# Performance work log

Hardware: AMD Instinct MI355X
Metric: run time of the kernel (lower is better)

## Reference

```python
import jax, jax.numpy as jnp
import numpy as np

EMBED_DIM = 1024
NUM_HEADS = 16
HEAD_DIM = EMBED_DIM // NUM_HEADS


def setup_inputs() -> dict:
    key = jax.random.key(0)
    ks = jax.random.split(key, 8)
    B, S, D = 2, 2048, EMBED_DIM
    scale = 1.0 / np.sqrt(D)
    return {
        "query": jax.random.normal(ks[0], (B, S, D), dtype=jnp.float32),
        "key": jax.random.normal(ks[1], (B, S, D), dtype=jnp.float32),
        "value": jax.random.normal(ks[2], (B, S, D), dtype=jnp.float32),
        "Wq": jax.random.normal(ks[3], (D, D), dtype=jnp.float32) * scale,
        "Wk": jax.random.normal(ks[4], (D, D), dtype=jnp.float32) * scale,
        "Wv": jax.random.normal(ks[5], (D, D), dtype=jnp.float32) * scale,
        "Wo": jax.random.normal(ks[6], (D, D), dtype=jnp.float32) * scale,
        "attention_mask": jax.random.randint(ks[7], (B, S), 0, 2, dtype=jnp.int32),
    }


def reference(query, key, value, Wq, Wk, Wv, Wo, attention_mask):
    B, Sq, D = query.shape
    Sk = key.shape[1]
    H, hd = NUM_HEADS, HEAD_DIM
    # linear projections (no bias), split into heads: [B, H, S, hd]
    q = (query @ Wq).reshape(B, Sq, H, hd).transpose(0, 2, 1, 3)
    k = (key @ Wk).reshape(B, Sk, H, hd).transpose(0, 2, 1, 3)
    v = (value @ Wv).reshape(B, Sk, H, hd).transpose(0, 2, 1, 3)
    # scaled dot-product scores: [B, H, Sq, Sk]; scale uses head_dim (post-split key dim)
    scores = jnp.einsum("bhqd,bhkd->bhqk", q, k) / jnp.sqrt(jnp.float32(hd))
    # padding mask [B, Sk] broadcast to [B, 1, 1, Sk]; 0 -> -inf
    mask = attention_mask[:, None, None, :]
    scores = jnp.where(mask == 0, -jnp.inf, scores)
    weights = jax.nn.softmax(scores, axis=-1)
    out = jnp.einsum("bhqk,bhkd->bhqd", weights, v)  # [B, H, Sq, hd]
    out = out.transpose(0, 2, 1, 3).reshape(B, Sq, D)
    return out @ Wo
```

## Files before the change

kernel.cpp:

```cpp
#include <hip/hip_runtime.h>
#include <hip/hip_bf16.h>

typedef short bf16x8 __attribute__((ext_vector_type(8)));
typedef float f32x4 __attribute__((ext_vector_type(4)));

#define S_LEN 2048
#define NHEAD 16
#define DM 1024

#if __has_builtin(__builtin_amdgcn_exp2f)
#define EXP2(x) __builtin_amdgcn_exp2f(x)
#else
#define EXP2(x) exp2f(x)
#endif

__device__ __forceinline__ short f2bf(float f) {
  union { float f; unsigned u; } x; x.f = f;
  unsigned r = x.u + 0x7fffu + ((x.u >> 16) & 1u);
  return (short)(r >> 16);
}

__device__ __forceinline__ unsigned cvt_pk_bf16(float lo, float hi) {
  unsigned r;
  asm("v_cvt_pk_bf16_f32 %0, %1, %2" : "=v"(r) : "v"(lo), "v"(hi));
  return r;
}

__device__ __forceinline__ void pl32swap(unsigned& a, unsigned& b) {
#if __has_builtin(__builtin_amdgcn_permlane32_swap)
  auto r = __builtin_amdgcn_permlane32_swap(a, b, false, false);
  a = r[0]; b = r[1];
#else
  asm volatile("v_permlane32_swap_b32 %0, %1" : "+v"(a), "+v"(b));
#endif
}
__device__ __forceinline__ void pl16swap(unsigned& a, unsigned& b) {
#if __has_builtin(__builtin_amdgcn_permlane16_swap)
  auto r = __builtin_amdgcn_permlane16_swap(a, b, false, false);
  a = r[0]; b = r[1];
#else
  asm volatile("v_permlane16_swap_b32 %0, %1" : "+v"(a), "+v"(b));
#endif
}

__device__ __forceinline__ void gload16(const void* g, void* l) {
  __builtin_amdgcn_global_load_lds(
      (const __attribute__((address_space(1))) void*)g,
      (__attribute__((address_space(3))) void*)l, 16, 0, 0);
}

__global__ __launch_bounds__(256) void wtrans(const float* __restrict__ Wq, const float* __restrict__ Wk,
                                              const float* __restrict__ Wv, const float* __restrict__ Wo,
                                              const int* __restrict__ mask,
                                              short* Tq, short* Tk, short* Tv, short* To, short* Mb) {
  const int z = blockIdx.z;
  const int tid = threadIdx.x;
  if (z == 4) {
    if (blockIdx.y == 0 && blockIdx.x < 16) {
      int i = blockIdx.x * 256 + tid;
      Mb[i] = mask[i] ? (short)0x3F80 : (short)0;
    }
    return;
  }
  const float* W = (z == 0) ? Wq : (z == 1) ? Wk : (z == 2) ? Wv : Wo;
  short* T = (z == 0) ? Tq : (z == 1) ? Tk : (z == 2) ? Tv : To;
  __shared__ short Tl[64][72];
  const int k0 = blockIdx.x * 64, n0 = blockIdx.y * 64;
  const int r = tid >> 2, c0 = (tid & 3) * 16;
#pragma unroll
  for (int j = 0; j < 4; j++) {
    float4 v = *(const float4*)&W[(size_t)(k0 + r) * DM + n0 + c0 + 4 * j];
    Tl[r][c0 + 4 * j + 0] = f2bf(v.x);
    Tl[r][c0 + 4 * j + 1] = f2bf(v.y);
    Tl[r][c0 + 4 * j + 2] = f2bf(v.z);
    Tl[r][c0 + 4 * j + 3] = f2bf(v.w);
  }
  __syncthreads();
  bf16x8 o0, o1;
#pragma unroll
  for (int j = 0; j < 8; j++) { o0[j] = Tl[c0 + j][r]; o1[j] = Tl[c0 + 8 + j][r]; }
  *(bf16x8*)&T[(size_t)(n0 + r) * DM + k0 + c0] = o0;
  *(bf16x8*)&T[(size_t)(n0 + r) * DM + k0 + c0 + 8] = o1;
}

__global__ __launch_bounds__(256) void xcvt(const float* __restrict__ q, const float* __restrict__ k,
                                            const float* __restrict__ v,
                                            short* xq, short* xk, short* xv) {
  const int z = blockIdx.y;
  const float* src = (z == 0) ? q : (z == 1) ? k : v;
  short* dst = (z == 0) ? xq : (z == 1) ? xk : xv;
  const size_t base = ((size_t)blockIdx.x * 256 + threadIdx.x) * 16;
  float4 a = *(const float4*)&src[base];
  float4 b = *(const float4*)&src[base + 4];
  float4 c = *(const float4*)&src[base + 8];
  float4 d = *(const float4*)&src[base + 12];
  bf16x8 o0, o1;
  o0[0] = f2bf(a.x); o0[1] = f2bf(a.y); o0[2] = f2bf(a.z); o0[3] = f2bf(a.w);
  o0[4] = f2bf(b.x); o0[5] = f2bf(b.y); o0[6] = f2bf(b.z); o0[7] = f2bf(b.w);
  o1[0] = f2bf(c.x); o1[1] = f2bf(c.y); o1[2] = f2bf(c.z); o1[3] = f2bf(c.w);
  o1[4] = f2bf(d.x); o1[5] = f2bf(d.y); o1[6] = f2bf(d.z); o1[7] = f2bf(d.w);
  *(bf16x8*)&dst[base] = o0;
  *(bf16x8*)&dst[base + 8] = o1;
}

template<int CM>
__global__ __launch_bounds__(256) void gemm3(const short* __restrict__ A, const short* __restrict__ Bt,
                                             void* __restrict__ Cp, int M, int N, int K,
                                             const int* __restrict__ mask) {
  __shared__ __align__(16) short Al[2][128 * 64];
  __shared__ __align__(16) short Bl[2][64 * 64];
  const int tid = threadIdx.x;
  const int lane = tid & 63, w = tid >> 6;
  const int wm = w >> 1, wn = w & 1;
  const int lr = lane & 15, g = lane >> 4;

  const int flat = blockIdx.y * gridDim.x + blockIdx.x;
  const int nwg = gridDim.x * gridDim.y;
  const int wid = (flat & 7) * (nwg >> 3) + (flat >> 3);
  const int bx = wid % gridDim.x, by = wid / gridDim.x;
  const int m0 = by * 128, n0 = bx * 64;

  f32x4 acc[4][2];
#pragma unroll
  for (int i = 0; i < 4; i++)
#pragma unroll
    for (int j = 0; j < 2; j++) acc[i][j] = (f32x4){0.f, 0.f, 0.f, 0.f};

  const int srow = lane >> 3;
  const int sch = (lane & 7) ^ (srow & 7);
  const short* gA = A + (size_t)(m0 + w * 32 + srow) * K + 8 * sch;
  const short* gB = Bt + (size_t)(n0 + w * 16 + srow) * K + 8 * sch;

#define STAGE(buf, kk)                                                              \
  do {                                                                              \
    _Pragma("unroll") for (int c = 0; c < 4; c++)                                   \
        gload16(gA + (size_t)c * 8 * K + (kk), &Al[buf][(w * 32 + c * 8) * 64]);    \
    _Pragma("unroll") for (int c = 0; c < 2; c++)                                   \
        gload16(gB + (size_t)c * 8 * K + (kk), &Bl[buf][(w * 16 + c * 8) * 64]);    \
  } while (0)

  const int nsteps = K >> 6;
  STAGE(0, 0);
  int buf = 0;
  for (int t = 0; t < nsteps; t++) {
    __syncthreads();
    if (t + 1 < nsteps) STAGE(buf ^ 1, (t + 1) << 6);
#pragma unroll
    for (int kc = 0; kc < 2; kc++) {
      bf16x8 af[4], bfr[2];
#pragma unroll
      for (int mt = 0; mt < 4; mt++) {
        int row = wm * 64 + mt * 16 + lr;
        af[mt] = *(const bf16x8*)&Al[buf][row * 64 + 8 * ((kc * 4 + g) ^ (lr & 7))];
      }
#pragma unroll
      for (int nt = 0; nt < 2; nt++) {
        int row = wn * 32 + nt * 16 + lr;
        bfr[nt] = *(const bf16x8*)&Bl[buf][row * 64 + 8 * ((kc * 4 + g) ^ (lr & 7))];
      }
      __builtin_amdgcn_s_setprio(1);
#pragma unroll
      for (int mt = 0; mt < 4; mt++)
#pragma unroll
        for (int nt = 0; nt < 2; nt++)
          acc[mt][nt] = __builtin_amdgcn_mfma_f32_16x16x32_bf16(af[mt], bfr[nt], acc[mt][nt], 0, 0, 0);
      __builtin_amdgcn_s_setprio(0);
    }
    buf ^= 1;
  }
#undef STAGE

#pragma unroll
  for (int mt = 0; mt < 4; mt++)
#pragma unroll
    for (int nt = 0; nt < 2; nt++) {
      if (CM == 0) {
#pragma unroll
        for (int r = 0; r < 4; r++) {
          int row = m0 + wm * 64 + mt * 16 + g * 4 + r;
          int col = n0 + wn * 32 + nt * 16 + lr;
          ((float*)Cp)[(size_t)row * N + col] = acc[mt][nt][r];
        }
      } else if (CM == 1 || CM == 3) {
        const float scale = (CM == 3) ? 0.18033688011f : 1.f;
#pragma unroll
        for (int r = 0; r < 4; r++) {
          int row = m0 + wm * 64 + mt * 16 + g * 4 + r;
          int col = n0 + wn * 32 + nt * 16 + lr;
          int b = row >> 11, s = row & (S_LEN - 1);
          int h = col >> 6, d = col & 63;
          ((short*)Cp)[(((size_t)(b * NHEAD + h)) * S_LEN + s) * 64 + d] = f2bf(acc[mt][nt][r] * scale);
        }
      } else {
#pragma unroll
        for (int r = 0; r < 4; r++) {
          int row = m0 + wm * 64 + mt * 16 + g * 4 + r;
          int col = n0 + wn * 32 + nt * 16 + lr;
          int h = row >> 6, d = row & 63;
          int b = col >> 11, s = col & (S_LEN - 1);
          float v = acc[mt][nt][r];
          if (CM == 4) v = mask[b * S_LEN + s] ? v : 0.f;
          ((short*)Cp)[(((size_t)(b * NHEAD + h)) * 64 + d) * S_LEN + s] = f2bf(v);
        }
      }
    }
}

template<int AM, int BMODE, int CM>
__global__ __launch_bounds__(256) void gemm2(const void* __restrict__ Ap, const void* __restrict__ Bp,
                                             void* __restrict__ Cp, int M, int N, int K) {
  __shared__ __align__(16) short Al[128][72];
  __shared__ __align__(16) short Bl[64][72];
  const int tid = threadIdx.x;
  const int lane = tid & 63, w = tid >> 6;
  const int wm = w >> 1, wn = w & 1;
  const int lr = lane & 15, g = lane >> 4;
  const int m0 = blockIdx.y * 128, n0 = blockIdx.x * 64;

  f32x4 acc[4][2];
#pragma unroll
  for (int i = 0; i < 4; i++)
// ... 68 lines not shown
      for (int j = 0; j < 2; j++) *(bf16x8*)&Bl[br][bc + 8 * j] = lb8[j];
    } else {
#pragma unroll
      for (int j = 0; j < 4; j++) {
        float4 v = lb[j];
        Bl[bc + 4 * j + 0][br] = f2bf(v.x);
        Bl[bc + 4 * j + 1][br] = f2bf(v.y);
        Bl[bc + 4 * j + 2][br] = f2bf(v.z);
        Bl[bc + 4 * j + 3][br] = f2bf(v.w);
      }
    }
    __syncthreads();
    if (t + 1 < nsteps) { LOADA((t + 1) << 6); LOADB((t + 1) << 6); }
#pragma unroll
    for (int kc = 0; kc < 2; kc++) {
      bf16x8 af[4], bfr[2];
#pragma unroll
      for (int mt = 0; mt < 4; mt++) af[mt] = *(const bf16x8*)&Al[wm * 64 + mt * 16 + lr][kc * 32 + g * 8];
#pragma unroll
      for (int nt = 0; nt < 2; nt++) bfr[nt] = *(const bf16x8*)&Bl[wn * 32 + nt * 16 + lr][kc * 32 + g * 8];
#pragma unroll
      for (int mt = 0; mt < 4; mt++)
#pragma unroll
        for (int nt = 0; nt < 2; nt++)
          acc[mt][nt] = __builtin_amdgcn_mfma_f32_16x16x32_bf16(af[mt], bfr[nt], acc[mt][nt], 0, 0, 0);
    }
  }
#undef LOADA
#undef LOADB

#pragma unroll
  for (int mt = 0; mt < 4; mt++)
#pragma unroll
    for (int nt = 0; nt < 2; nt++)
#pragma unroll
      for (int r = 0; r < 4; r++) {
        int row = m0 + wm * 64 + mt * 16 + g * 4 + r;
        int col = n0 + wn * 32 + nt * 16 + lr;
        if (CM == 0) {
          ((float*)Cp)[(size_t)row * N + col] = acc[mt][nt][r];
        } else if (CM == 1 || CM == 3) {
          float v = (CM == 3) ? acc[mt][nt][r] * 0.18033688011f : acc[mt][nt][r];
          int b = row >> 11, s = row & (S_LEN - 1);
          int h = col >> 6, d = col & 63;
          ((short*)Cp)[(((size_t)(b * NHEAD + h)) * S_LEN + s) * 64 + d] = f2bf(v);
        } else {
          int h = row >> 6, d = row & 63;
          int b = col >> 11, s = col & (S_LEN - 1);
          ((short*)Cp)[(((size_t)(b * NHEAD + h)) * 64 + d) * S_LEN + s] = f2bf(acc[mt][nt][r]);
        }
      }
}

__global__ __launch_bounds__(256, 4) void attn8(const short* __restrict__ Qb,
                                                const short* __restrict__ Kb,
                                                const short* __restrict__ VbT,
                                                const short* __restrict__ Mb,
                                                short* __restrict__ Ob) {
  __shared__ __align__(16) short Kl[2][64][64];
  __shared__ __align__(16) short Vl[2][64][64];

  const int tid = threadIdx.x;
  const int lane = tid & 63, w = tid >> 6;
  const int lr = lane & 15, g = lane >> 4;

  const int flat = blockIdx.y * gridDim.x + blockIdx.x;
  const int wid = (flat & 7) * 128 + (flat >> 3);
  const int qblk = wid & 31, bh = wid >> 5;
  const int b = bh >> 4, h = bh & 15;
  const int qbase = qblk * 64;
  const size_t hoff = (size_t)bh * S_LEN * 64;

  bf16x8 qf[2];
#pragma unroll
  for (int kh = 0; kh < 2; kh++)
    qf[kh] = *(const bf16x8*)&Qb[hoff + (size_t)(qbase + w * 16 + lr) * 64 + kh * 32 + g * 8];

  f32x4 o_acc[4];
  f32x4 o_l = (f32x4){0.f, 0.f, 0.f, 0.f};
#pragma unroll
  for (int dg = 0; dg < 4; dg++) o_acc[dg] = (f32x4){0.f, 0.f, 0.f, 0.f};

  const short* Mbb = Mb + b * S_LEN;
  const int srow = lane >> 3;
  const int sch = (lane & 7) ^ (srow & 7);
  const short* gK = Kb + hoff + (size_t)(w * 16 + srow) * 64 + 8 * sch;
  const short* gV = VbT + hoff + (size_t)(w * 16 + srow) * S_LEN + 8 * sch;

#define STAGEKV(buf, kb)                                                         \
  do {                                                                           \
    _Pragma("unroll") for (int c = 0; c < 2; c++)                                \
        gload16(gK + (size_t)(kb + c * 8) * 64, &Kl[buf][w * 16 + c * 8][0]);    \
    _Pragma("unroll") for (int c = 0; c < 2; c++)                                \
        gload16(gV + (size_t)c * 8 * S_LEN + (kb), &Vl[buf][w * 16 + c * 8][0]); \
  } while (0)

  const int NT = S_LEN / 64;
  STAGEKV(0, 0);
  int buf = 0;

  for (int t = 0; t < NT; t++) {
    const int kb = t * 64;
    bf16x8 mf0 = *(const bf16x8*)&Mbb[kb + g * 8];
    bf16x8 mf1 = *(const bf16x8*)&Mbb[kb + 32 + g * 8];
    __syncthreads();
    if (t + 1 < NT) STAGEKV(buf ^ 1, kb + 64);

    f32x4 s[4];
#pragma unroll
    for (int nt = 0; nt < 4; nt++) s[nt] = (f32x4){0.f, 0.f, 0.f, 0.f};
    __builtin_amdgcn_s_setprio(1);
#pragma unroll
    for (int nt = 0; nt < 4; nt++) {
      bf16x8 k0 = *(const bf16x8*)&Kl[buf][nt * 16 + lr][8 * (g ^ (lr & 7))];
      bf16x8 k1 = *(const bf16x8*)&Kl[buf][nt * 16 + lr][8 * ((4 + g) ^ (lr & 7))];
      s[nt] = __builtin_amdgcn_mfma_f32_16x16x32_bf16(k0, qf[0], s[nt], 0, 0, 0);
      s[nt] = __builtin_amdgcn_mfma_f32_16x16x32_bf16(k1, qf[1], s[nt], 0, 0, 0);
    }
    __builtin_amdgcn_s_setprio(0);

    unsigned W0[4], W1[4];
#pragma unroll
    for (int nt = 0; nt < 4; nt++) {
      float p0 = EXP2(s[nt][0]);
      float p1 = EXP2(s[nt][1]);
      float p2 = EXP2(s[nt][2]);
      float p3 = EXP2(s[nt][3]);
      W0[nt] = cvt_pk_bf16(p0, p1);
      W1[nt] = cvt_pk_bf16(p2, p3);
    }

    bf16x8 pf[2];
#pragma unroll
    for (int kh = 0; kh < 2; kh++) {
      unsigned a0 = W0[2 * kh], b0 = W0[2 * kh + 1];
      unsigned a1 = W1[2 * kh], b1 = W1[2 * kh + 1];
      pl32swap(a0, b0); pl16swap(a0, b0);
      pl32swap(a1, b1); pl16swap(a1, b1);
      union { unsigned u[4]; bf16x8 v; } pk;
      pk.u[0] = a0; pk.u[1] = a1; pk.u[2] = b0; pk.u[3] = b1;
      pf[kh] = pk.v;
    }

    __builtin_amdgcn_s_setprio(1);
#pragma unroll
    for (int dg = 0; dg < 4; dg++) {
      bf16x8 v0 = *(const bf16x8*)&Vl[buf][dg * 16 + lr][8 * (g ^ (lr & 7))];
      bf16x8 v1 = *(const bf16x8*)&Vl[buf][dg * 16 + lr][8 * ((4 + g) ^ (lr & 7))];
      o_acc[dg] = __builtin_amdgcn_mfma_f32_16x16x32_bf16(pf[0], v0, o_acc[dg], 0, 0, 0);
      o_acc[dg] = __builtin_amdgcn_mfma_f32_16x16x32_bf16(pf[1], v1, o_acc[dg], 0, 0, 0);
    }
    o_l = __builtin_amdgcn_mfma_f32_16x16x32_bf16(pf[0], mf0, o_l, 0, 0, 0);
    o_l = __builtin_amdgcn_mfma_f32_16x16x32_bf16(pf[1], mf1, o_l, 0, 0, 0);
    __builtin_amdgcn_s_setprio(0);
    buf ^= 1;
  }
#undef STAGEKV

#pragma unroll
  for (int r = 0; r < 4; r++) {
    float inv = 1.f / o_l[r];
    int qr = qbase + w * 16 + 4 * g + r;
#pragma unroll
    for (int dg = 0; dg < 4; dg++) {
      int col = h * 64 + dg * 16 + lr;
      Ob[((size_t)b * S_LEN + qr) * DM + col] = f2bf(o_acc[dg][r] * inv);
    }
  }
}

__global__ __launch_bounds__(256, 4) void attn7(const short* __restrict__ Qb,
                                                const short* __restrict__ Kb,
                                                const short* __restrict__ VbT,
                                                const int* __restrict__ mask,
                                                short* __restrict__ Ob) {
  __shared__ __align__(16) short Kl[2][64][64];
  __shared__ __align__(16) short Vl[2][64][64];

  const int tid = threadIdx.x;
  const int lane = tid & 63, w = tid >> 6;
  const int lr = lane & 15, g = lane >> 4;

  const int flat = blockIdx.y * gridDim.x + blockIdx.x;
  const int wid = (flat & 7) * 128 + (flat >> 3);
  const int qblk = wid & 31, bh = wid >> 5;
  const int b = bh >> 4, h = bh & 15;
  const int qbase = qblk * 64;
  const size_t hoff = (size_t)bh * S_LEN * 64;

  bf16x8 qf[2];
#pragma unroll
  for (int kh = 0; kh < 2; kh++)
    qf[kh] = *(const bf16x8*)&Qb[hoff + (size_t)(qbase + w * 16 + lr) * 64 + kh * 32 + g * 8];

  f32x4 o_acc[4];
  float lsum = 0.f;
#pragma unroll
  for (int dg = 0; dg < 4; dg++) o_acc[dg] = (f32x4){0.f, 0.f, 0.f, 0.f};

  const int* maskb = mask + b * S_LEN;
  const int srow = lane >> 3;
  const int sch = (lane & 7) ^ (srow & 7);
  const short* gK = Kb + hoff + (size_t)(w * 16 + srow) * 64 + 8 * sch;
  const short* gV = VbT + hoff + (size_t)(w * 16 + srow) * S_LEN + 8 * sch;

#define STAGEKV(buf, kb)                                                         \
  do {                                                                           \
    _Pragma("unroll") for (int c = 0; c < 2; c++)                                \
        gload16(gK + (size_t)(kb + c * 8) * 64, &Kl[buf][w * 16 + c * 8][0]);    \
    _Pragma("unroll") for (int c = 0; c < 2; c++)                                \
        gload16(gV + (size_t)c * 8 * S_LEN + (kb), &Vl[buf][w * 16 + c * 8][0]); \
  } while (0)

  const int NT = S_LEN / 64;
  STAGEKV(0, 0);
  int buf = 0;

  for (int t = 0; t < NT; t++) {
    const int kb = t * 64;
    __syncthreads();
// ... 42 lines not shown
      pl32swap(a0, b0); pl16swap(a0, b0);
      pl32swap(a1, b1); pl16swap(a1, b1);
      union { unsigned u[4]; bf16x8 v; } pk;
      pk.u[0] = a0; pk.u[1] = a1; pk.u[2] = b0; pk.u[3] = b1;
      pf[kh] = pk.v;
    }

    __builtin_amdgcn_s_setprio(1);
#pragma unroll
    for (int dg = 0; dg < 4; dg++) {
      bf16x8 v0 = *(const bf16x8*)&Vl[buf][dg * 16 + lr][8 * (g ^ (lr & 7))];
      bf16x8 v1 = *(const bf16x8*)&Vl[buf][dg * 16 + lr][8 * ((4 + g) ^ (lr & 7))];
      o_acc[dg] = __builtin_amdgcn_mfma_f32_16x16x32_bf16(pf[0], v0, o_acc[dg], 0, 0, 0);
      o_acc[dg] = __builtin_amdgcn_mfma_f32_16x16x32_bf16(pf[1], v1, o_acc[dg], 0, 0, 0);
    }
    __builtin_amdgcn_s_setprio(0);
    buf ^= 1;
  }
#undef STAGEKV

  {
    float l = lsum;
    l += __shfl_xor(l, 16);
    l += __shfl_xor(l, 32);
    float inv = 1.f / l;
    float invq[4];
#pragma unroll
    for (int r = 0; r < 4; r++) invq[r] = __shfl(inv, 4 * g + r);
#pragma unroll
    for (int dg = 0; dg < 4; dg++)
#pragma unroll
      for (int r = 0; r < 4; r++) {
        int qr = qbase + w * 16 + 4 * g + r;
        int col = h * 64 + dg * 16 + lr;
        Ob[((size_t)b * S_LEN + qr) * DM + col] = f2bf(o_acc[dg][r] * invq[r]);
      }
  }
}

extern "C" void kernel_launch(void* const* d_in, const int* in_sizes, int n_in,
                              void* d_out, int out_size, void* d_ws, size_t ws_size,
                              hipStream_t stream) {
  const float* query = (const float*)d_in[0];
  const float* key   = (const float*)d_in[1];
  const float* value = (const float*)d_in[2];
  const float* Wq = (const float*)d_in[3];
  const float* Wk = (const float*)d_in[4];
  const float* Wv = (const float*)d_in[5];
  const float* Wo = (const float*)d_in[6];
  const int* mask = (const int*)d_in[7];

  char* ws = (char*)d_ws;
  const size_t MB = 1 << 20;
  const bool big = ws_size >= 41 * MB;

  dim3 ag(S_LEN / 64, 2 * NHEAD);

  if (big) {
    short* xq  = (short*)(ws);
    short* xk  = (short*)(ws + 8 * MB);
    short* xv  = (short*)(ws + 16 * MB);
    short* WqT = (short*)(ws + 24 * MB);
    short* WkT = (short*)(ws + 26 * MB);
    short* WvT = (short*)(ws + 28 * MB);
    short* WoT = (short*)(ws + 30 * MB);
    short* Qb  = (short*)(ws + 32 * MB);
    short* Mb  = (short*)(ws + 40 * MB);
    short* Kb  = xq;
    short* VbT = xk;
    short* Ob  = xv;

    dim3 tgrid(16, 16, 5);
    wtrans<<<tgrid, 256, 0, stream>>>(Wq, Wk, Wv, Wo, mask, WqT, WkT, WvT, WoT, Mb);
    dim3 cg(1024, 3);
    xcvt<<<cg, 256, 0, stream>>>(query, key, value, xq, xk, xv);

    dim3 gqk(DM / 64, (2 * S_LEN) / 128);
    gemm3<3><<<gqk, 256, 0, stream>>>(xq, WqT, Qb, 2 * S_LEN, DM, DM, mask);
    gemm3<1><<<gqk, 256, 0, stream>>>(xk, WkT, Kb, 2 * S_LEN, DM, DM, mask);
    dim3 gv((2 * S_LEN) / 64, DM / 128);
    gemm3<4><<<gv, 256, 0, stream>>>(WvT, xv, VbT, DM, 2 * S_LEN, DM, mask);

    attn8<<<ag, 256, 0, stream>>>(Qb, Kb, VbT, Mb, Ob);

    gemm3<0><<<gqk, 256, 0, stream>>>(Ob, WoT, (float*)d_out, 2 * S_LEN, DM, DM, mask);
  } else {
    short* Qb  = (short*)(ws);
    short* Kb  = (short*)(ws + 8 * MB);
    short* VbT = (short*)(ws + 16 * MB);
    short* WqT = (short*)(ws + 24 * MB);
    short* WkT = (short*)(ws + 26 * MB);
    short* WvT = (short*)(ws + 28 * MB);
    short* Ob  = (short*)(ws + 24 * MB);

    dim3 tgrid(16, 16, 3);
    wtrans<<<tgrid, 256, 0, stream>>>(Wq, Wk, Wv, Wo, mask, WqT, WkT, WvT, WqT, WqT);

    dim3 gq(DM / 64, (2 * S_LEN) / 128);
    gemm2<0, 1, 3><<<gq, 256, 0, stream>>>(query, WqT, Qb, 2 * S_LEN, DM, DM);
    gemm2<0, 1, 1><<<gq, 256, 0, stream>>>(key,   WkT, Kb, 2 * S_LEN, DM, DM);
    dim3 gv((2 * S_LEN) / 64, DM / 128);
    gemm2<1, 0, 2><<<gv, 256, 0, stream>>>(WvT, value, VbT, DM, 2 * S_LEN, DM);

    attn7<<<ag, 256, 0, stream>>>(Qb, Kb, VbT, mask, Ob);

    gemm2<1, 2, 0><<<gq, 256, 0, stream>>>(Ob, Wo, (float*)d_out, 2 * S_LEN, DM, DM);
  }
}
```

Before: 138.5 us.

## Split attention over key halves with atomic accumulation, normalize inside output GEMM

Adds attn9, which gives each block 256 query rows and one half of the key range. Blocks accumulate unnormalized outputs and softmax denominators into fp32 buffers with atomicAdd, after those buffers are zeroed by memsets. A new gemmM kernel reads the fp32 partial sums, divides by the denominator, converts to bf16 in LDS and multiplies by Wo. The aim is more parallelism and more Q reuse per block, at the cost of atomic traffic, extra memsets and fp32 intermediates. It also relies on exp2 without max subtraction, as the earlier kernels did.

```diff
diff --git a/kernel.cpp b/kernel.cpp
--- a/kernel.cpp
+++ b/kernel.cpp
@@ -47,6 +47,12 @@
   __builtin_amdgcn_global_load_lds(
       (const __attribute__((address_space(1))) void*)g,
       (__attribute__((address_space(3))) void*)l, 16, 0, 0);
+}
+
+__device__ __forceinline__ float* op_row(float* p0, float* p1, float* p2, int tok) {
+  if (tok < 2048) return p0 + (size_t)tok * 1024;
+  if (tok < 3584) return p1 + (size_t)(tok - 2048) * 1024;
+  return p2 + (size_t)(tok - 3584) * 1024;
 }
 
 __global__ __launch_bounds__(256) void wtrans(const float* __restrict__ Wq, const float* __restrict__ Wk,
@@ -341,6 +347,245 @@
       }
 }
 
+__global__ __launch_bounds__(256, 2) void attn9(const short* __restrict__ Qb,
+                                                const short* __restrict__ Kb,
+                                                const short* __restrict__ VbT,
+                                                const short* __restrict__ Mb,
+                                                float* __restrict__ op0, float* __restrict__ op1,
+                                                float* __restrict__ op2, float* __restrict__ Lp) {
+  __shared__ __align__(16) short Kl[2][64][64];
+  __shared__ __align__(16) short Vl[2][64][64];
+
+  const int tid = threadIdx.x;
+  const int lane = tid & 63, w = tid >> 6;
+  const int lr = lane & 15, g = lane >> 4;
+
+  const int flat = blockIdx.y * gridDim.x + blockIdx.x;
+  const int wid = (flat & 7) * 64 + (flat >> 3);
+  const int qblk = wid & 7, half = (wid >> 3) & 1, bh = wid >> 4;
+  const int b = bh >> 4, h = bh & 15;
+  const int qbase = qblk * 256;
+  const int kb0 = half * 1024;
+  const size_t hoff = (size_t)bh * S_LEN * 64;
+
+  bf16x8 qf[4][2];
+#pragma unroll
+  for (int qfr = 0; qfr < 4; qfr++)
+#pragma unroll
+    for (int kh = 0; kh < 2; kh++)
+      qf[qfr][kh] = *(const bf16x8*)&Qb[hoff + (size_t)(qbase + w * 64 + qfr * 16 + lr) * 64 + kh * 32 + g * 8];
+
+  f32x4 o_acc[4][4];
+  f32x4 o_l[4];
+#pragma unroll
+  for (int qfr = 0; qfr < 4; qfr++) {
+    o_l[qfr] = (f32x4){0.f, 0.f, 0.f, 0.f};
+#pragma unroll
+    for (int dg = 0; dg < 4; dg++) o_acc[qfr][dg] = (f32x4){0.f, 0.f, 0.f, 0.f};
+  }
+
+  const short* Mbb = Mb + b * S_LEN;
+  const int srow = lane >> 3;
+  const int sch = (lane & 7) ^ (srow & 7);
+  const short* gK = Kb + hoff + (size_t)(w * 16 + srow) * 64 + 8 * sch;
+  const short* gV = VbT + hoff + (size_t)(w * 16 + srow) * S_LEN + 8 * sch;
+
+#define STAGEKV(buf, kb)                                                         \
+  do {                                                                           \
+    _Pragma("unroll") for (int c = 0; c < 2; c++)                                \
+        gload16(gK + (size_t)(kb + c * 8) * 64, &Kl[buf][w * 16 + c * 8][0]);    \
+    _Pragma("unroll") for (int c = 0; c < 2; c++)                                \
+        gload16(gV + (size_t)c * 8 * S_LEN + (kb), &Vl[buf][w * 16 + c * 8][0]); \
+  } while (0)
+
+  const int NT = 1024 / 64;
+  STAGEKV(0, kb0);
+  int buf = 0;
+
+  for (int t = 0; t < NT; t++) {
+    const int kb = kb0 + t * 64;
+    bf16x8 mf0 = *(const bf16x8*)&Mbb[kb + g * 8];
+    bf16x8 mf1 = *(const bf16x8*)&Mbb[kb + 32 + g * 8];
+    __syncthreads();
+    if (t + 1 < NT) STAGEKV(buf ^ 1, kb + 64);
+
+    bf16x8 kfr[4][2], vfr[4][2];
+#pragma unroll
+    for (int nt = 0; nt < 4; nt++)
+#pragma unroll
+      for (int kh = 0; kh < 2; kh++)
+        kfr[nt][kh] = *(const bf16x8*)&Kl[buf][nt * 16 + lr][8 * ((4 * kh + g) ^ (lr & 7))];
+#pragma unroll
+    for (int dg = 0; dg < 4; dg++)
+#pragma unroll
+      for (int kh = 0; kh < 2; kh++)
+        vfr[dg][kh] = *(const bf16x8*)&Vl[buf][dg * 16 + lr][8 * ((4 * kh + g) ^ (lr & 7))];
+
+#pragma unroll
+    for (int qfr = 0; qfr < 4; qfr++) {
+      f32x4 s[4];
+#pragma unroll
+      for (int nt = 0; nt < 4; nt++) s[nt] = (f32x4){0.f, 0.f, 0.f, 0.f};
+      __builtin_amdgcn_s_setprio(1);
+#pragma unroll
+      for (int nt = 0; nt < 4; nt++) {
+        s[nt] = __builtin_amdgcn_mfma_f32_16x16x32_bf16(kfr[nt][0], qf[qfr][0], s[nt], 0, 0, 0);
+        s[nt] = __builtin_amdgcn_mfma_f32_16x16x32_bf16(kfr[nt][1], qf[qfr][1], s[nt], 0, 0, 0);
+      }
+      __builtin_amdgcn_s_setprio(0);
+
+      unsigned W0[4], W1[4];
+#pragma unroll
+      for (int nt = 0; nt < 4; nt++) {
+        float p0 = EXP2(s[nt][0]);
+        float p1 = EXP2(s[nt][1]);
+        float p2 = EXP2(s[nt][2]);
+        float p3 = EXP2(s[nt][3]);
+        W0[nt] = cvt_pk_bf16(p0, p1);
+        W1[nt] = cvt_pk_bf16(p2, p3);
+      }
+
+      bf16x8 pf[2];
+#pragma unroll
+      for (int kh = 0; kh < 2; kh++) {
+        unsigned a0 = W0[2 * kh], b0 = W0[2 * kh + 1];
+        unsigned a1 = W1[2 * kh], b1 = W1[2 * kh + 1];
+        pl32swap(a0, b0); pl16swap(a0, b0);
+        pl32swap(a1, b1); pl16swap(a1, b1);
+        union { unsigned u[4]; bf16x8 v; } pk;
+        pk.u[0] = a0; pk.u[1] = a1; pk.u[2] = b0; pk.u[3] = b1;
+        pf[kh] = pk.v;
+      }
+
+      __builtin_amdgcn_s_setprio(1);
+#pragma unroll
+      for (int dg = 0; dg < 4; dg++) {
+        o_acc[qfr][dg] = __builtin_amdgcn_mfma_f32_16x16x32_bf16(pf[0], vfr[dg][0], o_acc[qfr][dg], 0, 0, 0);
+        o_acc[qfr][dg] = __builtin_amdgcn_mfma_f32_16x16x32_bf16(pf[1], vfr[dg][1], o_acc[qfr][dg], 0, 0, 0);
+      }
+      o_l[qfr] = __builtin_amdgcn_mfma_f32_16x16x32_bf16(pf[0], mf0, o_l[qfr], 0, 0, 0);
+      o_l[qfr] = __builtin_amdgcn_mfma_f32_16x16x32_bf16(pf[1], mf1, o_l[qfr], 0, 0, 0);
+      __builtin_amdgcn_s_setprio(0);
+    }
+    buf ^= 1;
+  }
+#undef STAGEKV
+
+#pragma unroll
+  for (int qfr = 0; qfr < 4; qfr++)
+#pragma unroll
+    for (int r = 0; r < 4; r++) {
+      int qr = qbase + w * 64 + qfr * 16 + 4 * g + r;
+      int tok = b * S_LEN + qr;
+      float* row = op_row(op0, op1, op2, tok);
+#pragma unroll
+      for (int dg = 0; dg < 4; dg++)
+        atomicAdd(&row[h * 64 + dg * 16 + lr], o_acc[qfr][dg][r]);
+      if (lr == 0) atomicAdd(&Lp[(size_t)(b * NHEAD + h) * S_LEN + qr], o_l[qfr][r]);
+    }
+}
+
+__global__ __launch_bounds__(256) void gemmM(float* __restrict__ op0, float* __restrict__ op1,
+                                             float* __restrict__ op2, const float* __restrict__ Lp,
+                                             const short* __restrict__ WoT, float* __restrict__ out) {
+  __shared__ __align__(16) short Al[128 * 64];
+  __shared__ __align__(16) short Bl[2][64 * 64];
+  const int tid = threadIdx.x;
+  const int lane = tid & 63, w = tid >> 6;
+  const int wm = w >> 1, wn = w & 1;
+  const int lr = lane & 15, g = lane >> 4;
+
+  const int flat = blockIdx.y * gridDim.x + blockIdx.x;
+  const int wid = (flat & 7) * 64 + (flat >> 3);
+  const int bx = wid & 15, by = wid >> 4;
+  const int m0 = by * 128, n0 = bx * 64;
+
+  f32x4 acc[4][2];
+#pragma unroll
+  for (int i = 0; i < 4; i++)
+#pragma unroll
+    for (int j = 0; j < 2; j++) acc[i][j] = (f32x4){0.f, 0.f, 0.f, 0.f};
+
+  const int ar = tid >> 1, ac = (tid & 1) * 32;
+  const int tok = m0 + ar;
+  const float* arow = op_row(op0, op1, op2, tok);
+  const int b = tok >> 11, s = tok & (S_LEN - 1);
+
+  const int srow = lane >> 3;
+  const int sch = (lane & 7) ^ (srow & 7);
+  const short* gB = WoT + (size_t)(n0 + w * 16 + srow) * 1024 + 8 * sch;
+
+  float4 la[8];
+  float lv;
+#define LOADA(kk)                                                             \
+  do {                                                                        \
+    _Pragma("unroll") for (int j = 0; j < 8; j++)                             \
+        la[j] = *(const float4*)&arow[(kk) + ac + 4 * j];                     \
+    lv = Lp[(size_t)(b * NHEAD + ((kk) >> 6)) * S_LEN + s];                   \
+  } while (0)
+#define STAGEB(buf, kk)                                                             \
+  do {                                                                              \
+    _Pragma("unroll") for (int c = 0; c < 2; c++)                                   \
+        gload16(gB + (size_t)c * 8 * 1024 + (kk), &Bl[buf][(w * 16 + c * 8) * 64]); \
+  } while (0)
+
+  const int nsteps = 16;
+  LOADA(0);
+  STAGEB(0, 0);
+  int buf = 0;
+  for (int t = 0; t < nsteps; t++) {
+    __syncthreads();
+    const float inv = 1.f / lv;
+#pragma unroll
+    for (int j = 0; j < 4; j++) {
+      float4 v0 = la[2 * j], v1 = la[2 * j + 1];
+      bf16x8 tt;
+      tt[0] = f2bf(v0.x * inv); tt[1] = f2bf(v0.y * inv);
+      tt[2] = f2bf(v0.z * inv); tt[3] = f2bf(v0.w * inv);
+      tt[4] = f2bf(v1.x * inv); tt[5] = f2bf(v1.y * inv);
+      tt[6] = f2bf(v1.z * inv); tt[7] = f2bf(v1.w * inv);
+      *(bf16x8*)&Al[ar * 64 + 8 * (((ac >> 3) + j) ^ (ar & 7))] = tt;
+    }
+    __syncthreads();
+    if (t + 1 < nsteps) { STAGEB(buf ^ 1, (t + 1) << 6); LOADA((t + 1) << 6); }
+#pragma unroll
+    for (int kc = 0; kc < 2; kc++) {
+      bf16x8 af[4], bfr[2];
+#pragma unroll
+      for (int mt = 0; mt < 4; mt++) {
+        int row = wm * 64 + mt * 16 + lr;
+        af[mt] = *(const bf16x8*)&Al[row * 64 + 8 * ((kc * 4 + g) ^ (lr & 7))];
+      }
+#pragma unroll
+      for (int nt = 0; nt < 2; nt++) {
+        int row = wn * 32 + nt * 16 + lr;
+        bfr[nt] = *(const bf16x8*)&Bl[buf][row * 64 + 8 * ((kc * 4 + g) ^ (lr & 7))];
+      }
+      __builtin_amdgcn_s_setprio(1);
+#pragma unroll
+      for (int mt = 0; mt < 4; mt++)
+#pragma unroll
+        for (int nt = 0; nt < 2; nt++)
+          acc[mt][nt] = __builtin_amdgcn_mfma_f32_16x16x32_bf16(af[mt], bfr[nt], acc[mt][nt], 0, 0, 0);
+      __builtin_amdgcn_s_setprio(0);
+    }
+    buf ^= 1;
+  }
+#undef LOADA
+#undef STAGEB
+
+#pragma unroll
+  for (int mt = 0; mt < 4; mt++)
+#pragma unroll
+    for (int nt = 0; nt < 2; nt++)
+#pragma unroll
+      for (int r = 0; r < 4; r++) {
+        int row = m0 + wm * 64 + mt * 16 + g * 4 + r;
+        int col = n0 + wn * 32 + nt * 16 + lr;
+        out[(size_t)row * DM + col] = acc[mt][nt][r];
+      }
+}
+
 __global__ __launch_bounds__(256, 4) void attn8(const short* __restrict__ Qb,
                                                 const short* __restrict__ Kb,
                                                 const short* __restrict__ VbT,
@@ -603,11 +848,48 @@
 
   char* ws = (char*)d_ws;
   const size_t MB = 1 << 20;
-  const bool big = ws_size >= 41 * MB;
-
-  dim3 ag(S_LEN / 64, 2 * NHEAD);
-
-  if (big) {
+  const bool big2 = ws_size >= 43 * MB;
+  const bool big  = ws_size >= 41 * MB;
+
+  if (big2) {
+    short* xq  = (short*)(ws);
+    short* xk  = (short*)(ws + 8 * MB);
+    short* xv  = (short*)(ws + 16 * MB);
+    short* WoT = (short*)(ws + 24 * MB);
+    short* WqT = (short*)(ws + 26 * MB);
+    short* WkT = (short*)(ws + 28 * MB);
+    short* WvT = (short*)(ws + 30 * MB);
+    short* Qb  = (short*)(ws + 32 * MB);
+    short* Mb  = (short*)(ws + 40 * MB);
+    float* Lp  = (float*)(ws + 40 * MB + 64 * 1024);
+    float* op0 = (float*)(ws + 16 * MB);
+    float* op1 = (float*)(ws + 26 * MB);
+    float* op2 = (float*)(ws + 41 * MB);
+    short* Kb  = xq;
+    short* VbT = xk;
+
+    dim3 tgrid(16, 16, 5);
+    wtrans<<<tgrid, 256, 0, stream>>>(Wq, Wk, Wv, Wo, mask, WqT, WkT, WvT, WoT, Mb);
+    dim3 cg(1024, 3);
+    xcvt<<<cg, 256, 0, stream>>>(query, key, value, xq, xk, xv);
+
+    dim3 gqk(DM / 64, (2 * S_LEN) / 128);
+    gemm3<3><<<gqk, 256, 0, stream>>>(xq, WqT, Qb, 2 * S_LEN, DM, DM, mask);
+    gemm3<1><<<gqk, 256, 0, stream>>>(xk, WkT, Kb, 2 * S_LEN, DM, DM, mask);
+    dim3 gv((2 * S_LEN) / 64, DM / 128);
+    gemm3<4><<<gv, 256, 0, stream>>>(WvT, xv, VbT, DM, 2 * S_LEN, DM, mask);
+
+    hipMemsetAsync(op0, 0, 8 * MB, stream);
+    hipMemsetAsync(op1, 0, 6 * MB, stream);
+    hipMemsetAsync(op2, 0, 2 * MB, stream);
+    hipMemsetAsync(Lp, 0, 2 * NHEAD * S_LEN * sizeof(float), stream);
+
+    dim3 ag(16, 32);
+    attn9<<<ag, 256, 0, stream>>>(Qb, Kb, VbT, Mb, op0, op1, op2, Lp);
+
+    dim3 go(16, 32);
+    gemmM<<<go, 256, 0, stream>>>(op0, op1, op2, Lp, WoT, (float*)d_out);
+  } else if (big) {
     short* xq  = (short*)(ws);
     short* xk  = (short*)(ws + 8 * MB);
     short* xv  = (short*)(ws + 16 * MB);
@@ -632,6 +914,7 @@
     dim3 gv((2 * S_LEN) / 64, DM / 128);
     gemm3<4><<<gv, 256, 0, stream>>>(WvT, xv, VbT, DM, 2 * S_LEN, DM, mask);
 
+    dim3 ag(S_LEN / 64, 2 * NHEAD);
     attn8<<<ag, 256, 0, stream>>>(Qb, Kb, VbT, Mb, Ob);
 
     gemm3<0><<<gqk, 256, 0, stream>>>(Ob, WoT, (float*)d_out, 2 * S_LEN, DM, DM, mask);
@@ -653,6 +936,7 @@
     dim3 gv((2 * S_LEN) / 64, DM / 128);
     gemm2<1, 0, 2><<<gv, 256, 0, stream>>>(WvT, value, VbT, DM, 2 * S_LEN, DM);
 
+    dim3 ag(S_LEN / 64, 2 * NHEAD);
     attn7<<<ag, 256, 0, stream>>>(Qb, Kb, VbT, mask, Ob);
 
     gemm2<1, 2, 0><<<gq, 256, 0, stream>>>(Ob, Wo, (float*)d_out, 2 * S_LEN, DM, DM);
```

Result: slower. 181.8 us (+31.3%).

## Triple-buffer GEMM and attention LDS pipelines with explicit vmcnt waits

Applied to the files above, without the earlier changes.

Converts the gemm3 and attention K/V shared-memory staging from double to triple buffering, prefetching two tiles ahead. A single barrier per step with a partial vmcnt wait replaces __syncthreads, so tile loads can stay in flight across iterations. The attention kernel also loads the padding-mask row into LDS once per block instead of reading it from global memory every iteration. The cost is more LDS per block (attention launch bounds drop from 4 to 3 blocks/CU), and correctness now depends on the hand-counted vmcnt values matching the number of issued loads.

```diff
diff --git a/kernel.cpp b/kernel.cpp
--- a/kernel.cpp
+++ b/kernel.cpp
@@ -107,8 +107,8 @@
 __global__ __launch_bounds__(256) void gemm3(const short* __restrict__ A, const short* __restrict__ Bt,
                                              void* __restrict__ Cp, int M, int N, int K,
                                              const int* __restrict__ mask) {
-  __shared__ __align__(16) short Al[2][128 * 64];
-  __shared__ __align__(16) short Bl[2][64 * 64];
+  __shared__ __align__(16) short Al[3][128 * 64];
+  __shared__ __align__(16) short Bl[3][64 * 64];
   const int tid = threadIdx.x;
   const int lane = tid & 63, w = tid >> 6;
   const int wm = w >> 1, wn = w & 1;
@@ -141,22 +141,28 @@
 
   const int nsteps = K >> 6;
   STAGE(0, 0);
-  int buf = 0;
+  STAGE(1, 64);
+  int cur = 0, sbuf = 2;
   for (int t = 0; t < nsteps; t++) {
-    __syncthreads();
-    if (t + 1 < nsteps) STAGE(buf ^ 1, (t + 1) << 6);
+    if (t < nsteps - 1)
+      asm volatile("s_waitcnt vmcnt(6) lgkmcnt(0)" ::: "memory");
+    else
+      asm volatile("s_waitcnt vmcnt(0) lgkmcnt(0)" ::: "memory");
+    __builtin_amdgcn_s_barrier();
+    __builtin_amdgcn_sched_barrier(0);
+    if (t + 2 < nsteps) STAGE(sbuf, (t + 2) << 6);
 #pragma unroll
     for (int kc = 0; kc < 2; kc++) {
       bf16x8 af[4], bfr[2];
 #pragma unroll
       for (int mt = 0; mt < 4; mt++) {
         int row = wm * 64 + mt * 16 + lr;
-        af[mt] = *(const bf16x8*)&Al[buf][row * 64 + 8 * ((kc * 4 + g) ^ (lr & 7))];
+        af[mt] = *(const bf16x8*)&Al[cur][row * 64 + 8 * ((kc * 4 + g) ^ (lr & 7))];
       }
 #pragma unroll
       for (int nt = 0; nt < 2; nt++) {
         int row = wn * 32 + nt * 16 + lr;
-        bfr[nt] = *(const bf16x8*)&Bl[buf][row * 64 + 8 * ((kc * 4 + g) ^ (lr & 7))];
+        bfr[nt] = *(const bf16x8*)&Bl[cur][row * 64 + 8 * ((kc * 4 + g) ^ (lr & 7))];
       }
       __builtin_amdgcn_s_setprio(1);
 #pragma unroll
@@ -166,7 +172,8 @@
           acc[mt][nt] = __builtin_amdgcn_mfma_f32_16x16x32_bf16(af[mt], bfr[nt], acc[mt][nt], 0, 0, 0);
       __builtin_amdgcn_s_setprio(0);
     }
-    buf ^= 1;
+    cur = (cur == 2) ? 0 : cur + 1;
+    sbuf = (sbuf == 2) ? 0 : sbuf + 1;
   }
 #undef STAGE
 
@@ -341,13 +348,14 @@
       }
 }
 
-__global__ __launch_bounds__(256, 4) void attn8(const short* __restrict__ Qb,
-                                                const short* __restrict__ Kb,
-                                                const short* __restrict__ VbT,
-                                                const short* __restrict__ Mb,
-                                                short* __restrict__ Ob) {
-  __shared__ __align__(16) short Kl[2][64][64];
-  __shared__ __align__(16) short Vl[2][64][64];
+__global__ __launch_bounds__(256, 3) void attn10(const short* __restrict__ Qb,
+                                                 const short* __restrict__ Kb,
+                                                 const short* __restrict__ VbT,
+                                                 const short* __restrict__ Mb,
+                                                 short* __restrict__ Ob) {
+  __shared__ __align__(16) short Kl[3][64][64];
+  __shared__ __align__(16) short Vl[3][64][64];
+  __shared__ __align__(16) short Ml[S_LEN];
 
   const int tid = threadIdx.x;
   const int lane = tid & 63, w = tid >> 6;
@@ -360,6 +368,8 @@
   const int qbase = qblk * 64;
   const size_t hoff = (size_t)bh * S_LEN * 64;
 
+  *(bf16x8*)&Ml[tid * 8] = *(const bf16x8*)&Mb[b * S_LEN + tid * 8];
+
   bf16x8 qf[2];
 #pragma unroll
   for (int kh = 0; kh < 2; kh++)
@@ -370,7 +380,6 @@
 #pragma unroll
   for (int dg = 0; dg < 4; dg++) o_acc[dg] = (f32x4){0.f, 0.f, 0.f, 0.f};
 
-  const short* Mbb = Mb + b * S_LEN;
   const int srow = lane >> 3;
   const int sch = (lane & 7) ^ (srow & 7);
   const short* gK = Kb + hoff + (size_t)(w * 16 + srow) * 64 + 8 * sch;
@@ -379,21 +388,28 @@
 #define STAGEKV(buf, kb)                                                         \
   do {                                                                           \
     _Pragma("unroll") for (int c = 0; c < 2; c++)                                \
-        gload16(gK + (size_t)(kb + c * 8) * 64, &Kl[buf][w * 16 + c * 8][0]);    \
+        gload16(gK + (size_t)((kb) + c * 8) * 64, &Kl[buf][w * 16 + c * 8][0]);  \
     _Pragma("unroll") for (int c = 0; c < 2; c++)                                \
         gload16(gV + (size_t)c * 8 * S_LEN + (kb), &Vl[buf][w * 16 + c * 8][0]); \
   } while (0)
 
   const int NT = S_LEN / 64;
   STAGEKV(0, 0);
-  int buf = 0;
+  STAGEKV(1, 64);
+  int cur = 0, sbuf = 2;
 
   for (int t = 0; t < NT; t++) {
     const int kb = t * 64;
-    bf16x8 mf0 = *(const bf16x8*)&Mbb[kb + g * 8];
-    bf16x8 mf1 = *(const bf16x8*)&Mbb[kb + 32 + g * 8];
-    __syncthreads();
-    if (t + 1 < NT) STAGEKV(buf ^ 1, kb + 64);
+    if (t < NT - 1)
+      asm volatile("s_waitcnt vmcnt(4) lgkmcnt(0)" ::: "memory");
+    else
+      asm volatile("s_waitcnt vmcnt(0) lgkmcnt(0)" ::: "memory");
+    __builtin_amdgcn_s_barrier();
+    __builtin_amdgcn_sched_barrier(0);
+    if (t + 2 < NT) STAGEKV(sbuf, kb + 128);
+
+    bf16x8 mf0 = *(const bf16x8*)&Ml[kb + g * 8];
+    bf16x8 mf1 = *(const bf16x8*)&Ml[kb + 32 + g * 8];
 
     f32x4 s[4];
 #pragma unroll
@@ -401,8 +417,8 @@
     __builtin_amdgcn_s_setprio(1);
 #pragma unroll
     for (int nt = 0; nt < 4; nt++) {
-      bf16x8 k0 = *(const bf16x8*)&Kl[buf][nt * 16 + lr][8 * (g ^ (lr & 7))];
-      bf16x8 k1 = *(const bf16x8*)&Kl[buf][nt * 16 + lr][8 * ((4 + g) ^ (lr & 7))];
+      bf16x8 k0 = *(const bf16x8*)&Kl[cur][nt * 16 + lr][8 * (g ^ (lr & 7))];
+      bf16x8 k1 = *(const bf16x8*)&Kl[cur][nt * 16 + lr][8 * ((4 + g) ^ (lr & 7))];
       s[nt] = __builtin_amdgcn_mfma_f32_16x16x32_bf16(k0, qf[0], s[nt], 0, 0, 0);
       s[nt] = __builtin_amdgcn_mfma_f32_16x16x32_bf16(k1, qf[1], s[nt], 0, 0, 0);
     }
@@ -434,15 +450,17 @@
     __builtin_amdgcn_s_setprio(1);
 #pragma unroll
     for (int dg = 0; dg < 4; dg++) {
-      bf16x8 v0 = *(const bf16x8*)&Vl[buf][dg * 16 + lr][8 * (g ^ (lr & 7))];
-      bf16x8 v1 = *(const bf16x8*)&Vl[buf][dg * 16 + lr][8 * ((4 + g) ^ (lr & 7))];
+      bf16x8 v0 = *(const bf16x8*)&Vl[cur][dg * 16 + lr][8 * (g ^ (lr & 7))];
+      bf16x8 v1 = *(const bf16x8*)&Vl[cur][dg * 16 + lr][8 * ((4 + g) ^ (lr & 7))];
       o_acc[dg] = __builtin_amdgcn_mfma_f32_16x16x32_bf16(pf[0], v0, o_acc[dg], 0, 0, 0);
       o_acc[dg] = __builtin_amdgcn_mfma_f32_16x16x32_bf16(pf[1], v1, o_acc[dg], 0, 0, 0);
     }
     o_l = __builtin_amdgcn_mfma_f32_16x16x32_bf16(pf[0], mf0, o_l, 0, 0, 0);
     o_l = __builtin_amdgcn_mfma_f32_16x16x32_bf16(pf[1], mf1, o_l, 0, 0, 0);
     __builtin_amdgcn_s_setprio(0);
-    buf ^= 1;
+
+    cur = (cur == 2) ? 0 : cur + 1;
+    sbuf = (sbuf == 2) ? 0 : sbuf + 1;
   }
 #undef STAGEKV
 
@@ -604,8 +622,6 @@
   char* ws = (char*)d_ws;
   const size_t MB = 1 << 20;
   const bool big = ws_size >= 41 * MB;
-
-  dim3 ag(S_LEN / 64, 2 * NHEAD);
 
   if (big) {
     short* xq  = (short*)(ws);
@@ -632,7 +648,8 @@
     dim3 gv((2 * S_LEN) / 64, DM / 128);
     gemm3<4><<<gv, 256, 0, stream>>>(WvT, xv, VbT, DM, 2 * S_LEN, DM, mask);
 
-    attn8<<<ag, 256, 0, stream>>>(Qb, Kb, VbT, Mb, Ob);
+    dim3 ag(S_LEN / 64, 2 * NHEAD);
+    attn10<<<ag, 256, 0, stream>>>(Qb, Kb, VbT, Mb, Ob);
 
     gemm3<0><<<gqk, 256, 0, stream>>>(Ob, WoT, (float*)d_out, 2 * S_LEN, DM, DM, mask);
   } else {
@@ -653,6 +670,7 @@
     dim3 gv((2 * S_LEN) / 64, DM / 128);
     gemm2<1, 0, 2><<<gv, 256, 0, stream>>>(WvT, value, VbT, DM, 2 * S_LEN, DM);
 
+    dim3 ag(S_LEN / 64, 2 * NHEAD);
     attn7<<<ag, 256, 0, stream>>>(Qb, Kb, VbT, mask, Ob);
 
     gemm2<1, 2, 0><<<gq, 256, 0, stream>>>(Ob, Wo, (float*)d_out, 2 * S_LEN, DM, DM);
```

Result: slower. 148.4 us (+7.2%).

## Split attention waves over query pairs and key halves with LDS reduction

Applied to the files above, without the earlier changes.

The attention kernel's four waves are reorganised as a 2x2 grid. Each wave now handles 32 query rows and half of every 64-key tile, so each K/V LDS fragment it loads feeds two query fragments. At the end, partial output and row-sum accumulators are combined through shared memory before normalising. The padding mask row is also staged once into LDS instead of being read from global memory every tile. In exchange the kernel uses more registers, lowers the launch-bounds occupancy hint from 4 to 3, and adds an epilogue reduction with extra barriers.

```diff
diff --git a/kernel.cpp b/kernel.cpp
--- a/kernel.cpp
+++ b/kernel.cpp
@@ -341,17 +341,19 @@
       }
 }
 
-__global__ __launch_bounds__(256, 4) void attn8(const short* __restrict__ Qb,
-                                                const short* __restrict__ Kb,
-                                                const short* __restrict__ VbT,
-                                                const short* __restrict__ Mb,
-                                                short* __restrict__ Ob) {
+__global__ __launch_bounds__(256, 3) void attn11(const short* __restrict__ Qb,
+                                                 const short* __restrict__ Kb,
+                                                 const short* __restrict__ VbT,
+                                                 const short* __restrict__ Mb,
+                                                 short* __restrict__ Ob) {
   __shared__ __align__(16) short Kl[2][64][64];
   __shared__ __align__(16) short Vl[2][64][64];
+  __shared__ __align__(16) short Ml[S_LEN];
 
   const int tid = threadIdx.x;
   const int lane = tid & 63, w = tid >> 6;
   const int lr = lane & 15, g = lane >> 4;
+  const int wq = w >> 1, wk = w & 1;
 
   const int flat = blockIdx.y * gridDim.x + blockIdx.x;
   const int wid = (flat & 7) * 128 + (flat >> 3);
@@ -360,17 +362,24 @@
   const int qbase = qblk * 64;
   const size_t hoff = (size_t)bh * S_LEN * 64;
 
-  bf16x8 qf[2];
-#pragma unroll
-  for (int kh = 0; kh < 2; kh++)
-    qf[kh] = *(const bf16x8*)&Qb[hoff + (size_t)(qbase + w * 16 + lr) * 64 + kh * 32 + g * 8];
-
-  f32x4 o_acc[4];
-  f32x4 o_l = (f32x4){0.f, 0.f, 0.f, 0.f};
-#pragma unroll
-  for (int dg = 0; dg < 4; dg++) o_acc[dg] = (f32x4){0.f, 0.f, 0.f, 0.f};
-
-  const short* Mbb = Mb + b * S_LEN;
+  *(bf16x8*)&Ml[tid * 8] = *(const bf16x8*)&Mb[b * S_LEN + tid * 8];
+
+  bf16x8 qf[2][2];
+#pragma unroll
+  for (int qfr = 0; qfr < 2; qfr++)
+#pragma unroll
+    for (int kh = 0; kh < 2; kh++)
+      qf[qfr][kh] = *(const bf16x8*)&Qb[hoff + (size_t)(qbase + wq * 32 + qfr * 16 + lr) * 64 + kh * 32 + g * 8];
+
+  f32x4 o_acc[2][4];
+  f32x4 o_l[2];
+#pragma unroll
+  for (int qfr = 0; qfr < 2; qfr++) {
+    o_l[qfr] = (f32x4){0.f, 0.f, 0.f, 0.f};
+#pragma unroll
+    for (int dg = 0; dg < 4; dg++) o_acc[qfr][dg] = (f32x4){0.f, 0.f, 0.f, 0.f};
+  }
+
   const int srow = lane >> 3;
   const int sch = (lane & 7) ^ (srow & 7);
   const short* gK = Kb + hoff + (size_t)(w * 16 + srow) * 64 + 8 * sch;
@@ -379,7 +388,7 @@
 #define STAGEKV(buf, kb)                                                         \
   do {                                                                           \
     _Pragma("unroll") for (int c = 0; c < 2; c++)                                \
-        gload16(gK + (size_t)(kb + c * 8) * 64, &Kl[buf][w * 16 + c * 8][0]);    \
+        gload16(gK + (size_t)((kb) + c * 8) * 64, &Kl[buf][w * 16 + c * 8][0]);  \
     _Pragma("unroll") for (int c = 0; c < 2; c++)                                \
         gload16(gV + (size_t)c * 8 * S_LEN + (kb), &Vl[buf][w * 16 + c * 8][0]); \
   } while (0)
@@ -390,71 +399,102 @@
 
   for (int t = 0; t < NT; t++) {
     const int kb = t * 64;
-    bf16x8 mf0 = *(const bf16x8*)&Mbb[kb + g * 8];
-    bf16x8 mf1 = *(const bf16x8*)&Mbb[kb + 32 + g * 8];
     __syncthreads();
     if (t + 1 < NT) STAGEKV(buf ^ 1, kb + 64);
 
-    f32x4 s[4];
-#pragma unroll
-    for (int nt = 0; nt < 4; nt++) s[nt] = (f32x4){0.f, 0.f, 0.f, 0.f};
-    __builtin_amdgcn_s_setprio(1);
-#pragma unroll
-    for (int nt = 0; nt < 4; nt++) {
-      bf16x8 k0 = *(const bf16x8*)&Kl[buf][nt * 16 + lr][8 * (g ^ (lr & 7))];
-      bf16x8 k1 = *(const bf16x8*)&Kl[buf][nt * 16 + lr][8 * ((4 + g) ^ (lr & 7))];
-      s[nt] = __builtin_amdgcn_mfma_f32_16x16x32_bf16(k0, qf[0], s[nt], 0, 0, 0);
-      s[nt] = __builtin_amdgcn_mfma_f32_16x16x32_bf16(k1, qf[1], s[nt], 0, 0, 0);
-    }
-    __builtin_amdgcn_s_setprio(0);
-
-    unsigned W0[4], W1[4];
-#pragma unroll
-    for (int nt = 0; nt < 4; nt++) {
-      float p0 = EXP2(s[nt][0]);
-      float p1 = EXP2(s[nt][1]);
-      float p2 = EXP2(s[nt][2]);
-      float p3 = EXP2(s[nt][3]);
-      W0[nt] = cvt_pk_bf16(p0, p1);
-      W1[nt] = cvt_pk_bf16(p2, p3);
-    }
-
-    bf16x8 pf[2];
-#pragma unroll
-    for (int kh = 0; kh < 2; kh++) {
-      unsigned a0 = W0[2 * kh], b0 = W0[2 * kh + 1];
-      unsigned a1 = W1[2 * kh], b1 = W1[2 * kh + 1];
-      pl32swap(a0, b0); pl16swap(a0, b0);
-      pl32swap(a1, b1); pl16swap(a1, b1);
-      union { unsigned u[4]; bf16x8 v; } pk;
-      pk.u[0] = a0; pk.u[1] = a1; pk.u[2] = b0; pk.u[3] = b1;
-      pf[kh] = pk.v;
-    }
-
-    __builtin_amdgcn_s_setprio(1);
-#pragma unroll
-    for (int dg = 0; dg < 4; dg++) {
-      bf16x8 v0 = *(const bf16x8*)&Vl[buf][dg * 16 + lr][8 * (g ^ (lr & 7))];
-      bf16x8 v1 = *(const bf16x8*)&Vl[buf][dg * 16 + lr][8 * ((4 + g) ^ (lr & 7))];
-      o_acc[dg] = __builtin_amdgcn_mfma_f32_16x16x32_bf16(pf[0], v0, o_acc[dg], 0, 0, 0);
-      o_acc[dg] = __builtin_amdgcn_mfma_f32_16x16x32_bf16(pf[1], v1, o_acc[dg], 0, 0, 0);
-    }
-    o_l = __builtin_amdgcn_mfma_f32_16x16x32_bf16(pf[0], mf0, o_l, 0, 0, 0);
-    o_l = __builtin_amdgcn_mfma_f32_16x16x32_bf16(pf[1], mf1, o_l, 0, 0, 0);
-    __builtin_amdgcn_s_setprio(0);
+    bf16x8 mf = *(const bf16x8*)&Ml[kb + wk * 32 + g * 8];
+
+    bf16x8 kfr[2][2];
+#pragma unroll
+    for (int nt = 0; nt < 2; nt++)
+#pragma unroll
+      for (int kh = 0; kh < 2; kh++)
+        kfr[nt][kh] = *(const bf16x8*)&Kl[buf][wk * 32 + nt * 16 + lr][8 * ((4 * kh + g) ^ (lr & 7))];
+
+    bf16x8 vfr[4];
+#pragma unroll
+    for (int dg = 0; dg < 4; dg++)
+      vfr[dg] = *(const bf16x8*)&Vl[buf][dg * 16 + lr][8 * ((4 * wk + g) ^ (lr & 7))];
+
+#pragma unroll
+    for (int qfr = 0; qfr < 2; qfr++) {
+      f32x4 s[2];
+#pragma unroll
+      for (int nt = 0; nt < 2; nt++) s[nt] = (f32x4){0.f, 0.f, 0.f, 0.f};
+      __builtin_amdgcn_s_setprio(1);
+#pragma unroll
+      for (int nt = 0; nt < 2; nt++) {
+        s[nt] = __builtin_amdgcn_mfma_f32_16x16x32_bf16(kfr[nt][0], qf[qfr][0], s[nt], 0, 0, 0);
+        s[nt] = __builtin_amdgcn_mfma_f32_16x16x32_bf16(kfr[nt][1], qf[qfr][1], s[nt], 0, 0, 0);
+      }
+      __builtin_amdgcn_s_setprio(0);
+
+      unsigned W0[2], W1[2];
+#pragma unroll
+      for (int nt = 0; nt < 2; nt++) {
+        float p0 = EXP2(s[nt][0]);
+        float p1 = EXP2(s[nt][1]);
+        float p2 = EXP2(s[nt][2]);
+        float p3 = EXP2(s[nt][3]);
+        W0[nt] = cvt_pk_bf16(p0, p1);
+        W1[nt] = cvt_pk_bf16(p2, p3);
+      }
+
+      bf16x8 pf;
+      {
+        unsigned a0 = W0[0], b0 = W0[1];
+        unsigned a1 = W1[0], b1 = W1[1];
+        pl32swap(a0, b0); pl16swap(a0, b0);
+        pl32swap(a1, b1); pl16swap(a1, b1);
+        union { unsigned u[4]; bf16x8 v; } pk;
+        pk.u[0] = a0; pk.u[1] = a1; pk.u[2] = b0; pk.u[3] = b1;
+        pf = pk.v;
+      }
+
+      __builtin_amdgcn_s_setprio(1);
+#pragma unroll
+      for (int dg = 0; dg < 4; dg++)
+        o_acc[qfr][dg] = __builtin_amdgcn_mfma_f32_16x16x32_bf16(pf, vfr[dg], o_acc[qfr][dg], 0, 0, 0);
+      o_l[qfr] = __builtin_amdgcn_mfma_f32_16x16x32_bf16(pf, mf, o_l[qfr], 0, 0, 0);
+      __builtin_amdgcn_s_setprio(0);
+    }
     buf ^= 1;
   }
 #undef STAGEKV
 
-#pragma unroll
-  for (int r = 0; r < 4; r++) {
-    float inv = 1.f / o_l[r];
-    int qr = qbase + w * 16 + 4 * g + r;
-#pragma unroll
-    for (int dg = 0; dg < 4; dg++) {
-      int col = h * 64 + dg * 16 + lr;
-      Ob[((size_t)b * S_LEN + qr) * DM + col] = f2bf(o_acc[dg][r] * inv);
-    }
+  __syncthreads();
+  float* Sf = (float*)&Kl[0][0][0];
+  float* Sl = (float*)&Vl[0][0][0];
+  if (wk == 1) {
+#pragma unroll
+    for (int qfr = 0; qfr < 2; qfr++) {
+#pragma unroll
+      for (int dg = 0; dg < 4; dg++)
+#pragma unroll
+        for (int r = 0; r < 4; r++)
+          Sf[(wq * 32 + qfr * 16 + 4 * g + r) * 64 + dg * 16 + lr] = o_acc[qfr][dg][r];
+      if (lr == 0)
+#pragma unroll
+        for (int r = 0; r < 4; r++)
+          Sl[wq * 32 + qfr * 16 + 4 * g + r] = o_l[qfr][r];
+    }
+  }
+  __syncthreads();
+  if (wk == 0) {
+#pragma unroll
+    for (int qfr = 0; qfr < 2; qfr++)
+#pragma unroll
+      for (int r = 0; r < 4; r++) {
+        int ql = wq * 32 + qfr * 16 + 4 * g + r;
+        float l = o_l[qfr][r] + Sl[ql];
+        float inv = 1.f / l;
+        int qr = qbase + ql;
+#pragma unroll
+        for (int dg = 0; dg < 4; dg++) {
+          float ov = o_acc[qfr][dg][r] + Sf[ql * 64 + dg * 16 + lr];
+          Ob[((size_t)b * S_LEN + qr) * DM + h * 64 + dg * 16 + lr] = f2bf(ov * inv);
+        }
+      }
   }
 }
 
@@ -604,8 +644,6 @@
   char* ws = (char*)d_ws;
   const size_t MB = 1 << 20;
   const bool big = ws_size >= 41 * MB;
-
-  dim3 ag(S_LEN / 64, 2 * NHEAD);
 
   if (big) {
     short* xq  = (short*)(ws);
@@ -632,7 +670,8 @@
     dim3 gv((2 * S_LEN) / 64, DM / 128);
     gemm3<4><<<gv, 256, 0, stream>>>(WvT, xv, VbT, DM, 2 * S_LEN, DM, mask);
 
-    attn8<<<ag, 256, 0, stream>>>(Qb, Kb, VbT, Mb, Ob);
+    dim3 ag(S_LEN / 64, 2 * NHEAD);
+    attn11<<<ag, 256, 0, stream>>>(Qb, Kb, VbT, Mb, Ob);
 
     gemm3<0><<<gqk, 256, 0, stream>>>(Ob, WoT, (float*)d_out, 2 * S_LEN, DM, DM, mask);
   } else {
@@ -653,6 +692,7 @@
     dim3 gv((2 * S_LEN) / 64, DM / 128);
     gemm2<1, 0, 2><<<gv, 256, 0, stream>>>(WvT, value, VbT, DM, 2 * S_LEN, DM);
 
+    dim3 ag(S_LEN / 64, 2 * NHEAD);
     attn7<<<ag, 256, 0, stream>>>(Qb, Kb, VbT, mask, Ob);
 
     gemm2<1, 2, 0><<<gq, 256, 0, stream>>>(Ob, Wo, (float*)d_out, 2 * S_LEN, DM, DM);
```

Measured after the change: 134.5 us. 1.03x faster.
